# Kernel optimization log

Measured on AMD Instinct MI355X. Metric: run time of the kernel, lower is better.

Reference implementation:

```python
import jax, jax.numpy as jnp
import numpy as np

D_MODEL = 1024
N_HEADS = 16
HEAD_DIM = D_MODEL // N_HEADS
BASE = 10000.0


def _rope_cos_sin(seq_len):
    # inv_freq: [head_dim/2]
    inv_freq = 1.0 / (BASE ** (jnp.arange(0, HEAD_DIM, 2, dtype=jnp.float32) / HEAD_DIM))
    t = jnp.arange(seq_len, dtype=jnp.float32)
    freqs = jnp.outer(t, inv_freq)                 # [S, head_dim/2]
    emb = jnp.concatenate([freqs, freqs], axis=-1)  # [S, head_dim]
    return jnp.cos(emb), jnp.sin(emb)


def _rotate_half(x):
    x1, x2 = jnp.split(x, 2, axis=-1)
    return jnp.concatenate([-x2, x1], axis=-1)


def setup_inputs() -> dict:
    key = jax.random.key(0)
    ks = jax.random.split(key, 9)
    B, S, D = 2, 2048, D_MODEL
    sc = 1.0 / np.sqrt(D)
    return {
        "x": jax.random.normal(ks[0], (B, S, D), jnp.float32),
        "Wq": jax.random.normal(ks[1], (D, D), jnp.float32) * sc,
        "bq": jax.random.normal(ks[2], (D,), jnp.float32) * 0.01,
        "Wk": jax.random.normal(ks[3], (D, D), jnp.float32) * sc,
        "bk": jax.random.normal(ks[4], (D,), jnp.float32) * 0.01,
        "Wv": jax.random.normal(ks[5], (D, D), jnp.float32) * sc,
        "bv": jax.random.normal(ks[6], (D,), jnp.float32) * 0.01,
        "Wo": jax.random.normal(ks[7], (D, D), jnp.float32) * sc,
        "bo": jax.random.normal(ks[8], (D,), jnp.float32) * 0.01,
    }


def reference(x, Wq, bq, Wk, bk, Wv, bv, Wo, bo):
    B, S, D = x.shape
    H, Hd = N_HEADS, HEAD_DIM
    # projections (torch Linear: x @ W.T + b), reshape to [B, H, S, Hd]
    def proj(W, b):
        y = jnp.einsum('bsd,ed->bse', x, W) + b
        return y.reshape(B, S, H, Hd).transpose(0, 2, 1, 3)
    q, k, v = proj(Wq, bq), proj(Wk, bk), proj(Wv, bv)
    cos, sin = _rope_cos_sin(S)            # [S, Hd]
    cos = cos[None, None]                   # [1,1,S,Hd]
    sin = sin[None, None]
    q = q * cos + _rotate_half(q) * sin
    k = k * cos + _rotate_half(k) * sin
    scale = jnp.sqrt(jnp.float32(Hd))
    scores = jnp.einsum('bhqd,bhkd->bhqk', q, k) / scale  # [B,H,S,S]
    attn = jax.nn.softmax(scores, axis=-1)
    out = jnp.einsum('bhqk,bhkd->bhqd', attn, v)          # [B,H,S,Hd]
    out = out.transpose(0, 2, 1, 3).reshape(B, S, D)
    return jnp.einsum('bsd,ed->bse', out, Wo) + bo
```

## Files before the change

kernel.cpp:

```cpp
#include <hip/hip_runtime.h>
#include <hip/hip_fp16.h>
#include <math.h>

#define D_MODEL 1024
#define NH 16
#define HD 64
#define SEQ 2048
#define BATCH 2
#define MROWS (BATCH*SEQ)
#define KDIM 1024

typedef unsigned short u16;
typedef __attribute__((ext_vector_type(8))) _Float16 h8;
typedef __attribute__((ext_vector_type(8))) short s8v;
typedef __attribute__((ext_vector_type(4))) float f4v;

#define MFMAH(a, b, c) __builtin_amdgcn_mfma_f32_16x16x32_f16(a, b, c, 0, 0, 0)

__device__ __forceinline__ void gld16(const u16* g, u16* l) {
    __builtin_amdgcn_global_load_lds(
        (const __attribute__((address_space(1))) void*)g,
        (__attribute__((address_space(3))) void*)l, 16, 0, 0);
}

__device__ __forceinline__ u16 f32_to_f16(float f) {
    return __half_as_ushort(__float2half(f));
}

__global__ __launch_bounds__(256)
void convert_f16(const float* __restrict__ x,
                 const float* __restrict__ Wq, const float* __restrict__ Wk,
                 const float* __restrict__ Wv, const float* __restrict__ Wo,
                 u16* __restrict__ xF,
                 u16* __restrict__ WqF, u16* __restrict__ WkF,
                 u16* __restrict__ WvF, u16* __restrict__ WoF,
                 float2* __restrict__ ropeT) {
    int i = blockIdx.x * 256 + threadIdx.x;
    if (i >= (1 << 20)) {
        int idx2 = i - (1 << 20);
        int s  = idx2 >> 5;
        int dd = idx2 & 31;
        float inv = __expf(-(float)dd * 0.2878231366f);
        float ang = (float)s * inv;
        ropeT[idx2] = make_float2(cosf(ang), sinf(ang));
        return;
    }
    const float* src;
    u16* dst;
    int idx;
    if (i < (1 << 19)) {
        src = x; dst = xF; idx = i;
    } else {
        int j = i - (1 << 19);
        int w = j >> 17;
        idx = j & ((1 << 17) - 1);
        switch (w) {
            case 0:  src = Wq; dst = WqF; break;
            case 1:  src = Wk; dst = WkF; break;
            case 2:  src = Wv; dst = WvF; break;
            default: src = Wo; dst = WoF; break;
        }
    }
    float4 a = ((const float4*)src)[idx * 2];
    float4 b = ((const float4*)src)[idx * 2 + 1];
    s8v o;
    o[0] = (short)f32_to_f16(a.x); o[1] = (short)f32_to_f16(a.y);
    o[2] = (short)f32_to_f16(a.z); o[3] = (short)f32_to_f16(a.w);
    o[4] = (short)f32_to_f16(b.x); o[5] = (short)f32_to_f16(b.y);
    o[6] = (short)f32_to_f16(b.z); o[7] = (short)f32_to_f16(b.w);
    ((s8v*)dst)[idx] = o;
}

__global__ __launch_bounds__(256, 2)
void qkv_gemm(const u16* __restrict__ xF, const u16* __restrict__ WqF,
              const u16* __restrict__ WkF, const u16* __restrict__ WvF,
              const float* __restrict__ bq, const float* __restrict__ bk,
              const float* __restrict__ bv,
              const float2* __restrict__ ropeT,
              u16* __restrict__ QF, u16* __restrict__ KF,
              u16* __restrict__ VtF, float* __restrict__ km2) {
    __shared__ __align__(16) u16 SMEM[32768];

    const int t    = threadIdx.x;
    const int w    = t >> 6;
    const int lane = t & 63;
    const int quad = lane >> 4;
    const int l15  = lane & 15;
    const int wr   = w >> 1;
    const int wc   = w & 1;

    const int bid  = blockIdx.x;
    const int xcd  = bid & 7;
    const int j    = bid >> 3;
    const int m0   = (xcd * 4 + (j & 3)) * 128;
    const int yt   = j >> 2;
    const int wsel = yt >> 3;
    const int n0   = (yt & 7) * 128;

    const u16* Bg;
    const float* bias;
    if (wsel == 0)      { Bg = WqF; bias = bq; }
    else if (wsel == 1) { Bg = WkF; bias = bk; }
    else                { Bg = WvF; bias = bv; }

    const int lr = lane >> 3;
    const int lc = (((lane & 7) ^ lr)) * 8;

    f4v acc[4][4];
    #pragma unroll
    for (int i = 0; i < 4; i++)
        #pragma unroll
        for (int jj = 0; jj < 4; jj++)
            acc[i][jj] = (f4v){0.f, 0.f, 0.f, 0.f};

#define STAGE(K0, DB) do {                                                   \
    u16* As_ = SMEM + (DB);                                                  \
    u16* Bs_ = As_ + 8192;                                                   \
    _Pragma("unroll")                                                        \
    for (int jj_ = 0; jj_ < 4; jj_++) {                                      \
        int seg = jj_ * 4 + w;                                               \
        gld16(xF + (size_t)(m0 + seg * 8 + lr) * KDIM + (K0) + lc,           \
              As_ + seg * 512);                                              \
        gld16(Bg + (size_t)(n0 + seg * 8 + lr) * KDIM + (K0) + lc,           \
              Bs_ + seg * 512);                                              \
    }                                                                        \
} while (0)

    STAGE(0, 0);
    __syncthreads();

    int buf = 0;
    for (int k0 = 0; k0 < KDIM; k0 += 64) {
        if (k0 + 64 < KDIM) STAGE(k0 + 64, (buf ^ 1) * 16384);

        const u16* As = SMEM + buf * 16384;
        const u16* Bs = As + 8192;
        #pragma unroll
        for (int kk = 0; kk < 2; kk++) {
            const int swz = ((kk * 4 + quad) ^ (l15 & 7)) << 3;
            h8 a[4], b[4];
            #pragma unroll
            for (int mt = 0; mt < 4; mt++)
                a[mt] = *(const h8*)&As[(wr * 64 + mt * 16 + l15) * 64 + swz];
            #pragma unroll
            for (int nt = 0; nt < 4; nt++)
                b[nt] = *(const h8*)&Bs[(wc * 64 + nt * 16 + l15) * 64 + swz];
            #pragma unroll
            for (int mt = 0; mt < 4; mt++)
                #pragma unroll
                for (int nt = 0; nt < 4; nt++)
                    acc[mt][nt] = MFMAH(a[mt], b[nt], acc[mt][nt]);
        }
        __syncthreads();
        buf ^= 1;
    }
#undef STAGE

    const int bb = m0 >> 11;
    const int s0 = m0 & 2047;
    const int h0 = n0 >> 6;

    if (wsel < 2) {
        u16* OF = (wsel == 0) ? QF : KF;
        float kn_max = 0.f;
        #pragma unroll
        for (int mt = 0; mt < 4; mt++) {
            #pragma unroll
            for (int r = 0; r < 4; r++) {
                int R = wr * 64 + mt * 16 + quad * 4 + r;
                int s = s0 + R;
                float rowsum = 0.f;
                #pragma unroll
                for (int nt = 0; nt < 2; nt++) {
                    int col = wc * 64 + nt * 16 + l15;
                    int n1 = n0 + col;
                    int dd = n1 & 31;
                    float v1 = acc[mt][nt][r]     + bias[n1];
                    float v2 = acc[mt][nt + 2][r] + bias[n1 + 32];
                    float2 cssn = ropeT[(s << 5) | dd];
                    float cs  = cssn.x;
                    float sn  = cssn.y;
                    float r1 = v1 * cs - v2 * sn;
                    float r2 = v2 * cs + v1 * sn;
                    rowsum += v1 * v1 + v2 * v2;
                    SMEM[R * 128 + (((col >> 3) ^ (R & 15)) << 3) + (col & 7)]
                        = f32_to_f16(r1);
                    int col2 = col + 32;
                    SMEM[R * 128 + (((col2 >> 3) ^ (R & 15)) << 3) + (col2 & 7)]
                        = f32_to_f16(r2);
                }
                if (wsel == 1) {
                    rowsum += __shfl_xor(rowsum, 1, 64);
                    rowsum += __shfl_xor(rowsum, 2, 64);
                    rowsum += __shfl_xor(rowsum, 4, 64);
                    rowsum += __shfl_xor(rowsum, 8, 64);
                    kn_max = fmaxf(kn_max, rowsum);
                }
            }
        }
        if (wsel == 1) {
            kn_max = fmaxf(kn_max, __shfl_xor(kn_max, 16, 64));
            kn_max = fmaxf(kn_max, __shfl_xor(kn_max, 32, 64));
            if (lane == 0) atomicMax((int*)km2, __float_as_int(kn_max));
        }
        __syncthreads();
        #pragma unroll
        for (int cc = 0; cc < 8; cc++) {
            int idx  = cc * 256 + t;
            int hl   = idx >> 10;
            int rem  = idx & 1023;
            int R    = rem >> 3;
            int dch  = rem & 7;
            s8v val = *(const s8v*)&SMEM[R * 128 +
                          (((hl * 8 + dch) ^ (R & 15)) << 3)];
            *(s8v*)(OF + (((size_t)bb * NH + h0 + hl) * SEQ + s0 + R) * 64
                       + dch * 8) = val;
        }
    } else {
        #pragma unroll
        for (int mt = 0; mt < 4; mt++) {
            #pragma unroll
            for (int nt = 0; nt < 4; nt++) {
                int n = wc * 64 + nt * 16 + l15;
                float bv_ = bias[n0 + n];
                #pragma unroll
                for (int r = 0; r < 4; r++) {
                    int m = wr * 64 + mt * 16 + quad * 4 + r;
                    float v = acc[mt][nt][r] + bv_;
                    SMEM[n * 128 + (((m >> 3) ^ (n & 15)) << 3) + (m & 7)]
                        = f32_to_f16(v);
                }
            }
        }
        __syncthreads();
        #pragma unroll
        for (int cc = 0; cc < 8; cc++) {
            int idx = cc * 256 + t;
            int n   = idx >> 4;
            int mc  = idx & 15;
            int d   = n & 63;
            int hh  = n >> 6;
            size_t obase = ((size_t)((bb * NH + h0 + hh) * HD + d)) * SEQ + s0;
            s8v val = *(const s8v*)&SMEM[n * 128 + ((mc ^ (n & 15)) << 3)];
            *(s8v*)(VtF + obase + mc * 8) = val;
        }
    }
}

__global__ __launch_bounds__(256, 4)
void flash_attn(const u16* __restrict__ QF, const u16* __restrict__ KF,
                const u16* __restrict__ VtF,
                const float* __restrict__ kmax2,
                u16* __restrict__ AOF) {
    __shared__ __align__(16) u16 KS[2][32 * 72];
    __shared__ __align__(16) u16 VtS[2][64 * 40];
    __shared__ __align__(16) u16 PS[64 * 36];

    const int t    = threadIdx.x;
    const int w    = t >> 6;
    const int lane = t & 63;
    const int quad = lane >> 4;
    const int l15  = lane & 15;

    const int bid = blockIdx.x;
    const int xcd = bid & 7;
    const int j   = bid >> 3;
    const int bh  = xcd * 4 + (j & 3);
    const int q0  = (j >> 2) * 64;

    const size_t kvbase = (size_t)bh * SEQ * HD;
    const float km2 = kmax2[0];

    h8 qf[2];
    float mb[4];
    {
        const u16* qp = QF + kvbase +
            (size_t)(q0 + w * 16 + l15) * HD + quad * 8;
        qf[0] = *(const h8*)qp;
        qf[1] = *(const h8*)(qp + 32);
        float qn2 = 0.f;
        #pragma unroll
        for (int st = 0; st < 2; st++)
            #pragma unroll
            for (int e = 0; e < 8; e++) {
                float v = (float)qf[st][e];
                qn2 += v * v;
            }
        qn2 += __shfl_xor(qn2, 16, 64);
        qn2 += __shfl_xor(qn2, 32, 64);
        #pragma unroll
        for (int r = 0; r < 4; r++) {
            int src = (lane & 48) | (quad * 4 + r);
            float qr = __shfl(qn2, src, 64);
            mb[r] = sqrtf(qr * km2) * 0.125f;
        }
    }

    f4v o[4];
    float lsum[4];
    #pragma unroll
    for (int nt = 0; nt < 4; nt++) {
        o[nt] = (f4v){0.f, 0.f, 0.f, 0.f};
        lsum[nt] = 0.f;
    }

    const int krow = t >> 3;
    const int kdc  = (t & 7) * 8;
    const u16* kgp = KF + kvbase + (size_t)krow * HD + kdc;
    const int vd   = t >> 2;
    const int vkc  = (t & 3) * 8;
    const int vcol = vkc ^ (((vd >> 3) & 3) << 3);
    const u16* vgp = VtF + (size_t)bh * HD * SEQ + (size_t)vd * SEQ + vkc;

    s8v krg0 = *(const s8v*)(kgp);
    s8v krg1 = *(const s8v*)(kgp + (size_t)32 * HD);
    s8v vrg0 = *(const s8v*)(vgp);
    s8v vrg1 = *(const s8v*)(vgp + 32);

    for (int k0 = 0; k0 < SEQ; k0 += 64) {
        __syncthreads();
        *(s8v*)&KS[0][krow * 72 + kdc] = krg0;
        *(s8v*)&KS[1][krow * 72 + kdc] = krg1;
        *(s8v*)&VtS[0][vd * 40 + vcol] = vrg0;
        *(s8v*)&VtS[1][vd * 40 + vcol] = vrg1;
        if (k0 + 64 < SEQ) {
            const u16* kn = kgp + (size_t)(k0 + 64) * HD;
            krg0 = *(const s8v*)(kn);
            krg1 = *(const s8v*)(kn + (size_t)32 * HD);
            vrg0 = *(const s8v*)(vgp + k0 + 64);
            vrg1 = *(const s8v*)(vgp + k0 + 96);
        }
        __syncthreads();

        #pragma unroll
        for (int sub = 0; sub < 2; sub++) {
            const u16* kb0 = KS[sub] + l15 * 72 + quad * 8;
            const u16* kb1 = KS[sub] + (16 + l15) * 72 + quad * 8;
            h8 kh0 = *(const h8*)kb0, kh1 = *(const h8*)(kb0 + 32);
            h8 kh2 = *(const h8*)kb1, kh3 = *(const h8*)(kb1 + 32);

            f4v sc0 = (f4v){0.f, 0.f, 0.f, 0.f};
            f4v sc1 = (f4v){0.f, 0.f, 0.f, 0.f};
            __builtin_amdgcn_s_setprio(1);
            sc0 = MFMAH(qf[0], kh0, sc0);
            sc0 = MFMAH(qf[1], kh1, sc0);
            sc1 = MFMAH(qf[0], kh2, sc1);
            sc1 = MFMAH(qf[1], kh3, sc1);
            __builtin_amdgcn_s_setprio(0);

            #pragma unroll
            for (int r = 0; r < 4; r++) {
                float p0 = __expf(sc0[r] * 0.125f - mb[r]);
                float p1 = __expf(sc1[r] * 0.125f - mb[r]);
                lsum[r] += p0 + p1;
                int row_l = w * 16 + quad * 4 + r;
                PS[row_l * 36 + l15]      = f32_to_f16(p0);
                PS[row_l * 36 + 16 + l15] = f32_to_f16(p1);
            }

            const int prow = w * 16 + l15;
            h8 ph = *(const h8*)&PS[prow * 36 + quad * 8];
            __builtin_amdgcn_s_setprio(1);
            #pragma unroll
            for (int nt = 0; nt < 4; nt++) {
                int dim = nt * 16 + l15;
                int voff = dim * 40 + ((quad * 8) ^ (((dim >> 3) & 3) << 3));
                o[nt] = MFMAH(ph, *(const h8*)&VtS[sub][voff], o[nt]);
            }
            __builtin_amdgcn_s_setprio(0);
        }
    }

    const int b = bh >> 4;
    const int h = bh & 15;
    #pragma unroll
    for (int r = 0; r < 4; r++) {
        float l = lsum[r];
        l += __shfl_xor(l, 1, 64);
        l += __shfl_xor(l, 2, 64);
        l += __shfl_xor(l, 4, 64);
        l += __shfl_xor(l, 8, 64);
        float inv_l = 1.0f / l;
        int s = q0 + w * 16 + quad * 4 + r;
        size_t obase = (((size_t)b * SEQ + s) * NH + h) * HD;
        #pragma unroll
        for (int nt = 0; nt < 4; nt++) {
            AOF[obase + nt * 16 + l15] = f32_to_f16(o[nt][r] * inv_l);
        }
    }
}

__global__ __launch_bounds__(256, 2)
void gemm_out(const u16* __restrict__ AF, const u16* __restrict__ BF,
              const float* __restrict__ bias, float* __restrict__ out) {
    __shared__ __align__(16) u16 SMEM[24576];

    const int t    = threadIdx.x;
    const int w    = t >> 6;
    const int lane = t & 63;
    const int quad = lane >> 4;
    const int l15  = lane & 15;
    const int wr   = w >> 1;
    const int wc   = w & 1;

    const int bid = blockIdx.x;
    const int xcd = bid & 7;
    const int j   = bid >> 3;
    const int m0  = (xcd * 4 + (j & 3)) * 128;
    const int n0  = (j >> 2) * 64;

    const int lr = lane >> 3;
    const int lc = (((lane & 7) ^ lr)) * 8;

    f4v acc[4][2];
    #pragma unroll
    for (int i = 0; i < 4; i++)
        #pragma unroll
        for (int jj = 0; jj < 2; jj++)
            acc[i][jj] = (f4v){0.f, 0.f, 0.f, 0.f};

#define STAGE(K0, DB) do {                                                   \
    u16* As_ = SMEM + (DB);                                                  \
    u16* Bs_ = As_ + 8192;                                                   \
    _Pragma("unroll")                                                        \
    for (int jj_ = 0; jj_ < 4; jj_++) {                                      \
        int seg = jj_ * 4 + w;                                               \
        gld16(AF + (size_t)(m0 + seg * 8 + lr) * KDIM + (K0) + lc,           \
              As_ + seg * 512);                                              \
    }                                                                        \
    _Pragma("unroll")                                                        \
    for (int jj_ = 0; jj_ < 2; jj_++) {                                      \
        int seg = jj_ * 4 + w;                                               \
        gld16(BF + (size_t)(n0 + seg * 8 + lr) * KDIM + (K0) + lc,           \
              Bs_ + seg * 512);                                              \
    }                                                                        \
} while (0)

    STAGE(0, 0);
    __syncthreads();

    int buf = 0;
    for (int k0 = 0; k0 < KDIM; k0 += 64) {
        if (k0 + 64 < KDIM) STAGE(k0 + 64, (buf ^ 1) * 12288);

        const u16* As = SMEM + buf * 12288;
        const u16* Bs = As + 8192;
        #pragma unroll
        for (int kk = 0; kk < 2; kk++) {
            const int swz = ((kk * 4 + quad) ^ (l15 & 7)) << 3;
            h8 a[4], b[2];
            #pragma unroll
            for (int mt = 0; mt < 4; mt++)
                a[mt] = *(const h8*)&As[(wr * 64 + mt * 16 + l15) * 64 + swz];
            #pragma unroll
            for (int nt = 0; nt < 2; nt++)
                b[nt] = *(const h8*)&Bs[(wc * 32 + nt * 16 + l15) * 64 + swz];
            #pragma unroll
            for (int mt = 0; mt < 4; mt++)
                #pragma unroll
                for (int nt = 0; nt < 2; nt++)
                    acc[mt][nt] = MFMAH(a[mt], b[nt], acc[mt][nt]);
        }
        __syncthreads();
        buf ^= 1;
    }
#undef STAGE

    #pragma unroll
    for (int mt = 0; mt < 4; mt++) {
        #pragma unroll
        for (int nt = 0; nt < 2; nt++) {
            int n = n0 + wc * 32 + nt * 16 + l15;
            float bv = bias[n];
            #pragma unroll
            for (int r = 0; r < 4; r++) {
                int m = m0 + wr * 64 + mt * 16 + quad * 4 + r;
                out[(size_t)m * 1024 + n] = acc[mt][nt][r] + bv;
            }
        }
    }
}

extern "C" void kernel_launch(void* const* d_in, const int* in_sizes, int n_in,
                              void* d_out, int out_size, void* d_ws, size_t ws_size,
                              hipStream_t stream) {
    const float* x  = (const float*)d_in[0];
    const float* Wq = (const float*)d_in[1];
    const float* bq = (const float*)d_in[2];
    const float* Wk = (const float*)d_in[3];
    const float* bk = (const float*)d_in[4];
    const float* Wv = (const float*)d_in[5];
    const float* bv = (const float*)d_in[6];
    const float* Wo = (const float*)d_in[7];
    const float* bo = (const float*)d_in[8];
    float* out = (float*)d_out;

    const size_t TEN = (size_t)MROWS * KDIM;
    const size_t WSZ = (size_t)KDIM * KDIM;

    u16* xF  = (u16*)d_ws;
    u16* WqF = xF + TEN;
    u16* WkF = WqF + WSZ;
    u16* WvF = WkF + WSZ;
    u16* WoF = WvF + WSZ;
    u16* QF  = WoF + WSZ;
    u16* KF  = QF + TEN;
    u16* VtF = KF + TEN;
    float* km2 = (float*)(VtF + TEN);
    float2* ropeT = (float2*)(km2 + 4);
    u16* AOF = xF;

    convert_f16<<<4352, 256, 0, stream>>>(x, Wq, Wk, Wv, Wo,
                                          xF, WqF, WkF, WvF, WoF, ropeT);

    hipMemsetAsync(km2, 0, 4, stream);

    qkv_gemm<<<768, 256, 0, stream>>>(xF, WqF, WkF, WvF,
                                      bq, bk, bv, ropeT, QF, KF, VtF, km2);

    flash_attn<<<1024, 256, 0, stream>>>(QF, KF, VtF, km2, AOF);

    gemm_out<<<512, 256, 0, stream>>>(AOF, WoF, bo, out);
}
```

Before: 223.5 us.

## Transpose attention MFMAs to keep P in registers and stage output through LDS

Swaps the MFMA operand order so the score tile comes out transposed, with each lane holding the probabilities for its own query row. The probabilities are then packed straight into the A operand of the PV MFMA, which removes the LDS round trip through the PS buffer and the per-row shuffles for the max bound and row sum. K rows are loaded in a permuted order so the register layout lines up with the PV operand. The epilogue now writes the output tile through swizzled LDS so global stores are 16-byte coalesced, at the cost of two extra barriers.

```diff
diff --git a/kernel.cpp b/kernel.cpp
--- a/kernel.cpp
+++ b/kernel.cpp
@@ -254,7 +254,6 @@
                 u16* __restrict__ AOF) {
     __shared__ __align__(16) u16 KS[2][32 * 72];
     __shared__ __align__(16) u16 VtS[2][64 * 40];
-    __shared__ __align__(16) u16 PS[64 * 36];
 
     const int t    = threadIdx.x;
     const int w    = t >> 6;
@@ -272,7 +271,7 @@
     const float km2 = kmax2[0];
 
     h8 qf[2];
-    float mb[4];
+    float mb;
     {
         const u16* qp = QF + kvbase +
             (size_t)(q0 + w * 16 + l15) * HD + quad * 8;
@@ -288,25 +287,18 @@
             }
         qn2 += __shfl_xor(qn2, 16, 64);
         qn2 += __shfl_xor(qn2, 32, 64);
-        #pragma unroll
-        for (int r = 0; r < 4; r++) {
-            int src = (lane & 48) | (quad * 4 + r);
-            float qr = __shfl(qn2, src, 64);
-            mb[r] = sqrtf(qr * km2) * 0.125f;
-        }
+        mb = sqrtf(qn2 * km2) * 0.125f;
     }
 
     f4v o[4];
-    float lsum[4];
     #pragma unroll
-    for (int nt = 0; nt < 4; nt++) {
-        o[nt] = (f4v){0.f, 0.f, 0.f, 0.f};
-        lsum[nt] = 0.f;
-    }
+    for (int nt = 0; nt < 4; nt++) o[nt] = (f4v){0.f, 0.f, 0.f, 0.f};
+    float lsum = 0.f;
 
     const int krow = t >> 3;
     const int kdc  = (t & 7) * 8;
-    const u16* kgp = KF + kvbase + (size_t)krow * HD + kdc;
+    const int pkey = (krow & 3) + 8 * ((krow >> 2) & 3) + 4 * (krow >> 4);
+    const u16* kgp = KF + kvbase + (size_t)pkey * HD + kdc;
     const int vd   = t >> 2;
     const int vkc  = (t & 3) * 8;
     const int vcol = vkc ^ (((vd >> 3) & 3) << 3);
@@ -342,51 +334,66 @@
             f4v sc0 = (f4v){0.f, 0.f, 0.f, 0.f};
             f4v sc1 = (f4v){0.f, 0.f, 0.f, 0.f};
             __builtin_amdgcn_s_setprio(1);
-            sc0 = MFMAH(qf[0], kh0, sc0);
-            sc0 = MFMAH(qf[1], kh1, sc0);
-            sc1 = MFMAH(qf[0], kh2, sc1);
-            sc1 = MFMAH(qf[1], kh3, sc1);
+            sc0 = MFMAH(kh0, qf[0], sc0);
+            sc0 = MFMAH(kh1, qf[1], sc0);
+            sc1 = MFMAH(kh2, qf[0], sc1);
+            sc1 = MFMAH(kh3, qf[1], sc1);
             __builtin_amdgcn_s_setprio(0);
 
+            float p[8];
             #pragma unroll
             for (int r = 0; r < 4; r++) {
-                float p0 = __expf(sc0[r] * 0.125f - mb[r]);
-                float p1 = __expf(sc1[r] * 0.125f - mb[r]);
-                lsum[r] += p0 + p1;
-                int row_l = w * 16 + quad * 4 + r;
-                PS[row_l * 36 + l15]      = f32_to_f16(p0);
-                PS[row_l * 36 + 16 + l15] = f32_to_f16(p1);
+                p[r]     = __expf(sc0[r] * 0.125f - mb);
+                p[4 + r] = __expf(sc1[r] * 0.125f - mb);
             }
-
-            const int prow = w * 16 + l15;
-            h8 ph = *(const h8*)&PS[prow * 36 + quad * 8];
+            lsum += ((p[0] + p[1]) + (p[2] + p[3]))
+                  + ((p[4] + p[5]) + (p[6] + p[7]));
+
+            h8 pb;
+            __half2* pp = (__half2*)&pb;
+            pp[0] = __floats2half2_rn(p[0], p[1]);
+            pp[1] = __floats2half2_rn(p[2], p[3]);
+            pp[2] = __floats2half2_rn(p[4], p[5]);
+            pp[3] = __floats2half2_rn(p[6], p[7]);
+
             __builtin_amdgcn_s_setprio(1);
             #pragma unroll
             for (int nt = 0; nt < 4; nt++) {
                 int dim = nt * 16 + l15;
                 int voff = dim * 40 + ((quad * 8) ^ (((dim >> 3) & 3) << 3));
-                o[nt] = MFMAH(ph, *(const h8*)&VtS[sub][voff], o[nt]);
+                o[nt] = MFMAH(*(const h8*)&VtS[sub][voff], pb, o[nt]);
             }
             __builtin_amdgcn_s_setprio(0);
         }
     }
 
+    lsum += __shfl_xor(lsum, 16, 64);
+    lsum += __shfl_xor(lsum, 32, 64);
+    float inv_l = 1.0f / lsum;
+
     const int b = bh >> 4;
     const int h = bh & 15;
+    u16* OS = &KS[0][0];
+    __syncthreads();
+    const int srow = w * 16 + l15;
     #pragma unroll
-    for (int r = 0; r < 4; r++) {
-        float l = lsum[r];
-        l += __shfl_xor(l, 1, 64);
-        l += __shfl_xor(l, 2, 64);
-        l += __shfl_xor(l, 4, 64);
-        l += __shfl_xor(l, 8, 64);
-        float inv_l = 1.0f / l;
-        int s = q0 + w * 16 + quad * 4 + r;
-        size_t obase = (((size_t)b * SEQ + s) * NH + h) * HD;
-        #pragma unroll
-        for (int nt = 0; nt < 4; nt++) {
-            AOF[obase + nt * 16 + l15] = f32_to_f16(o[nt][r] * inv_l);
-        }
+    for (int nt = 0; nt < 4; nt++) {
+        #pragma unroll
+        for (int r = 0; r < 4; r++) {
+            int d = nt * 16 + quad * 4 + r;
+            OS[srow * 64 + (((d >> 3) ^ (srow & 7)) << 3) + (d & 7)]
+                = f32_to_f16(o[nt][r] * inv_l);
+        }
+    }
+    __syncthreads();
+    #pragma unroll
+    for (int cc = 0; cc < 2; cc++) {
+        int idx = cc * 256 + t;
+        int sr  = idx >> 3;
+        int dch = idx & 7;
+        s8v val = *(const s8v*)&OS[sr * 64 + ((dch ^ (sr & 7)) << 3)];
+        *(s8v*)(AOF + (((size_t)b * SEQ + q0 + sr) * NH + h) * HD + dch * 8)
+            = val;
     }
 }
 
```

New measurement: 201.8 us. 9.7% less time.
